# Kernel optimization log

Measured on AMD Instinct MI355X. Metric: run time of the kernel, lower is better.

## Reference

```python
import jax, jax.numpy as jnp
import numpy as np
from jax import lax

B, E, V, T = 16384, 256, 128, 16
TAU = 1.0


def _gru(x, h, Wih, Whh, bih, bhh):
    # torch.nn.GRUCell math
    gi = x @ Wih.T + bih
    gh = h @ Whh.T + bhh
    ir, iz, i_n = jnp.split(gi, 3, axis=-1)
    hr, hz, h_n = jnp.split(gh, 3, axis=-1)
    r = jax.nn.sigmoid(ir + hr)
    z = jax.nn.sigmoid(iz + hz)
    n = jnp.tanh(i_n + r * h_n)
    return (1.0 - z) * n + z * h


def setup_inputs() -> dict:
    key = jax.random.key(0)
    ks = jax.random.split(key, 10)
    s = 0.05
    w = lambda k, shape: jax.random.normal(k, shape, jnp.float32) * s
    return {
        "x": jax.random.normal(ks[0], (B, E), jnp.float32),
        "global_idxes": jnp.arange(B, dtype=jnp.int32),
        "uniform_noise": jax.random.uniform(ks[1], (T, B, V), dtype=jnp.float32),
        "dec_Wd2e": w(ks[2], (E, V)), "dec_bd2e": jnp.zeros((E,), jnp.float32),
        "dec_Wih": w(ks[3], (3 * E, E)), "dec_Whh": w(ks[4], (3 * E, E)),
        "dec_bih": jnp.zeros((3 * E,), jnp.float32), "dec_bhh": jnp.zeros((3 * E,), jnp.float32),
        "dec_We2d": w(ks[5], (V, E)), "dec_be2d": jnp.zeros((V,), jnp.float32),
        "enc_Wd2e": w(ks[6], (E, V)), "enc_bd2e": jnp.zeros((E,), jnp.float32),
        "enc_Wih": w(ks[7], (3 * E, E)), "enc_Whh": w(ks[8], (3 * E, E)),
        "enc_bih": jnp.zeros((3 * E,), jnp.float32), "enc_bhh": jnp.zeros((3 * E,), jnp.float32),
    }


def _forward(x, uniform_noise,
             dec_Wd2e, dec_bd2e, dec_Wih, dec_Whh, dec_bih, dec_bhh, dec_We2d, dec_be2d,
             enc_Wd2e, enc_bd2e, enc_Wih, enc_Whh, enc_bih, enc_bhh):
    Bn = x.shape[0]
    # gumbel noise from pre-sampled uniforms (deterministic)
    gnoise = -jnp.log(-jnp.log(uniform_noise + 1e-10) + 1e-10)  # [T,B,V]

    # ---- GumbelDecoder: sequential GRUCell decode with alive/dead masking ----
    def dec_step(carry, g_t):
        state, last_tok, alive, N, t = carry
        emb = last_tok @ dec_Wd2e.T + dec_bd2e
        state = _gru(emb, state, dec_Wih, dec_Whh, dec_bih, dec_bhh)
        logits = state @ dec_We2d.T + dec_be2d
        y_soft = jax.nn.softmax((logits + g_t) / TAU, axis=-1)
        idx = jnp.argmax(y_soft, axis=-1)
        y_hard = jax.nn.one_hot(idx, V, dtype=y_soft.dtype)
        # straight-through hard gumbel-softmax
        y = y_soft + lax.stop_gradient(y_hard - y_soft)
        ended = idx == 0  # token 0 is the terminator
        N = jnp.where(ended, jnp.minimum(N, t), N)
        alive = alive & (~ended)
        # dead rows (incl. newly ended) have their token zeroed, as in torch
        y = jnp.where(alive[:, None], y, 0.0)
        return (state, y, alive, N, t + 1), y

    init = (x, jnp.zeros((Bn, V), x.dtype), jnp.ones((Bn,), bool),
            jnp.full((Bn,), T, jnp.int32), jnp.int32(0))
    (_, _, _, N, _), utt = lax.scan(dec_step, init, gnoise)  # utt: [T,B,V]

    # ---- OnehotEncoder: sequential GRUCell encode with alive sieve (masked) ----
    def enc_step(carry, u_t):
        state, out_state, alive = carry
        emb = u_t @ enc_Wd2e.T + enc_bd2e
        state = _gru(emb, state, enc_Wih, enc_Whh, enc_bih, enc_bhh)
        out_state = jnp.where(alive[:, None], state, out_state)
        ended = u_t[:, 0] > 0.5  # terminator seen in utterance
        alive = alive & (~ended)
        return (state, out_state, alive), None

    z0 = jnp.zeros((Bn, E), x.dtype)
    (_, reconst, _), _ = lax.scan(enc_step, (z0, z0, jnp.ones((Bn,), bool)), utt)

    utterance = jnp.transpose(utt, (1, 0, 2))  # [B,T,V]
    return utterance, N, reconst


def reference(x, global_idxes, uniform_noise,
              dec_Wd2e, dec_bd2e, dec_Wih, dec_Whh, dec_bih, dec_bhh, dec_We2d, dec_be2d,
              enc_Wd2e, enc_bd2e, enc_Wih, enc_Whh, enc_bih, enc_bhh):
    del global_idxes  # unused by the original forward
    return _forward(x, uniform_noise,
                    dec_Wd2e, dec_bd2e, dec_Wih, dec_Whh, dec_bih, dec_bhh, dec_We2d, dec_be2d,
                    enc_Wd2e, enc_bd2e, enc_Wih, enc_Whh, enc_bih, enc_bhh)
```

## Files before the change

### kernel.cpp

```cpp
#include <hip/hip_runtime.h>
#include <hip/hip_bf16.h>


namespace {
constexpr int kB  = 16384;
constexpr int kE  = 256;
constexpr int kV  = 128;
constexpr int kT  = 16;
constexpr int kG3 = 768;

constexpr int kOffWdhhT  = 0;
constexpr int kOffWehhT  = kG3 * kE;
constexpr int kOffWe2dT  = 2 * kG3 * kE;
constexpr int kOffDecTab = kOffWe2dT + kV * kE;
constexpr int kOffEncTab = kOffDecTab + 129 * kG3;
}

__device__ __forceinline__ float sigmf(float v) { return 1.0f / (1.0f + expf(-v)); }
__device__ __forceinline__ float gumbelf(float u) {
  return -logf(-logf(u + 1e-10f) + 1e-10f);
}

__global__ void prep_transpose(const float* __restrict__ dWhh,
                               const float* __restrict__ eWhh,
                               const float* __restrict__ We2d,
                               float* __restrict__ ws) {
  const int n1 = kG3 * kE;
  const int n2 = n1 + kG3 * kE;
  const int n3 = n2 + kV * kE;
  for (int i = blockIdx.x * blockDim.x + threadIdx.x; i < n3;
       i += gridDim.x * blockDim.x) {
    if (i < n1) {
      const int k = i / kG3, j = i - k * kG3;
      ws[i] = dWhh[j * kE + k];
    } else if (i < n2) {
      const int t = i - n1;
      const int k = t / kG3, j = t - k * kG3;
      ws[i] = eWhh[j * kE + k];
    } else {
      const int t = i - n2;
      const int k = t / kV, v = t - k * kV;
      ws[i] = We2d[v * kE + k];
    }
  }
}

__global__ void prep_tables(const float* __restrict__ Wih,
                            const float* __restrict__ Wd2e,
                            const float* __restrict__ bd2e,
                            const float* __restrict__ bih,
                            float* __restrict__ tab) {
  const int i = blockIdx.x * blockDim.x + threadIdx.x;
  if (i >= 129 * kG3) return;
  const int v = i / kG3, j = i - v * kG3;
  const float* wr = Wih + j * kE;
  float acc = 0.0f;
  if (v < kV) {
    for (int k = 0; k < kE; ++k) acc = fmaf(wr[k], Wd2e[k * kV + v] + bd2e[k], acc);
  } else {
    for (int k = 0; k < kE; ++k) acc = fmaf(wr[k], bd2e[k], acc);
  }
  tab[i] = acc + bih[j];
}

__device__ __forceinline__ void gru_half(float acc[8][3][4],
                                         const float (*__restrict__ h)[8],
                                         const float* __restrict__ WT,
                                         const int e0) {
#pragma unroll
  for (int r = 0; r < 8; ++r)
#pragma unroll
    for (int g = 0; g < 3; ++g)
#pragma unroll
      for (int c = 0; c < 4; ++c) acc[r][g][c] = 0.0f;
#pragma unroll 2
  for (int k = 0; k < kE; ++k) {
    const float4 hA = *(const float4*)(&h[k][0]);
    const float4 hB = *(const float4*)(&h[k][4]);
    const float* wp = WT + k * kG3 + e0;
    const float4 w0 = *(const float4*)(wp);
    const float4 w1 = *(const float4*)(wp + 256);
    const float4 w2 = *(const float4*)(wp + 512);
    const float hv[8] = {hA.x, hA.y, hA.z, hA.w, hB.x, hB.y, hB.z, hB.w};
    const float wv[3][4] = {{w0.x, w0.y, w0.z, w0.w},
                            {w1.x, w1.y, w1.z, w1.w},
                            {w2.x, w2.y, w2.z, w2.w}};
#pragma unroll
    for (int r = 0; r < 8; ++r)
#pragma unroll
      for (int g = 0; g < 3; ++g)
#pragma unroll
        for (int c = 0; c < 4; ++c)
          acc[r][g][c] = fmaf(hv[r], wv[g][c], acc[r][g][c]);
  }
}

__device__ __forceinline__ void gru_pointwise(float acc[8][3][4],
                                              float (*__restrict__ h)[8],
                                              const float* __restrict__ Tab,
                                              const int tok[8],
                                              const float4& br4, const float4& bz4,
                                              const float4& bn4, const int e0) {
  const float br[4] = {br4.x, br4.y, br4.z, br4.w};
  const float bz[4] = {bz4.x, bz4.y, bz4.z, bz4.w};
  const float bn[4] = {bn4.x, bn4.y, bn4.z, bn4.w};
#pragma unroll
  for (int r = 0; r < 8; ++r) {
    const float* gp = Tab + tok[r] * kG3 + e0;
    const float4 g0 = *(const float4*)(gp);
    const float4 g1 = *(const float4*)(gp + 256);
    const float4 g2 = *(const float4*)(gp + 512);
    const float gi[3][4] = {{g0.x, g0.y, g0.z, g0.w},
                            {g1.x, g1.y, g1.z, g1.w},
                            {g2.x, g2.y, g2.z, g2.w}};
#pragma unroll
    for (int c = 0; c < 4; ++c) {
      const float rg = sigmf(gi[0][c] + acc[r][0][c] + br[c]);
      const float zg = sigmf(gi[1][c] + acc[r][1][c] + bz[c]);
      const float ng = tanhf(gi[2][c] + rg * (acc[r][2][c] + bn[c]));
      acc[r][0][c] = ng;
      acc[r][1][c] = zg;
    }
  }
#pragma unroll
  for (int c = 0; c < 4; ++c) {
    const int e = e0 + c;
    const float4 hA = *(const float4*)(&h[e][0]);
    const float4 hB = *(const float4*)(&h[e][4]);
    const float ho[8] = {hA.x, hA.y, hA.z, hA.w, hB.x, hB.y, hB.z, hB.w};
    float hn[8];
#pragma unroll
    for (int r = 0; r < 8; ++r)
      hn[r] = (1.0f - acc[r][1][c]) * acc[r][0][c] + acc[r][1][c] * ho[r];
    *(float4*)(&h[e][0]) = make_float4(hn[0], hn[1], hn[2], hn[3]);
    *(float4*)(&h[e][4]) = make_float4(hn[4], hn[5], hn[6], hn[7]);
  }
}

__launch_bounds__(256, 2)
__global__ void gumbel_fused(const float* __restrict__ x,
                             const float* __restrict__ unoise,
                             const float* __restrict__ dbhh,
                             const float* __restrict__ dbe2d,
                             const float* __restrict__ ebhh,
                             const float* __restrict__ ws,
                             float* __restrict__ out) {
  const float* WdhhT  = ws + kOffWdhhT;
  const float* WehhT  = ws + kOffWehhT;
  const float* We2dT  = ws + kOffWe2dT;
  const float* DecTab = ws + kOffDecTab;
  const float* EncTab = ws + kOffEncTab;

  __shared__ float hbuf[2][4][kE][8];

  const int tid  = (int)threadIdx.x;
  const int w    = tid >> 6;
  const int jx   = tid & 63;
  const int row0 = (int)blockIdx.x * 32 + w * 8;
  const int e0   = jx * 4;

  float (*hd)[8] = hbuf[0][w];
  float (*he)[8] = hbuf[1][w];

  for (int i = jx; i < kE * 8; i += 64) {
    const int r = i >> 8, k = i & (kE - 1);
    hd[k][r] = x[(size_t)(row0 + r) * kE + k];
    he[k][r] = 0.0f;
  }
  __syncthreads();

  int tok[8], Nn[8];
  bool alive[8];
#pragma unroll
  for (int r = 0; r < 8; ++r) { tok[r] = kV; Nn[r] = kT; alive[r] = true; }

  const float4 dbr = *(const float4*)(dbhh + e0);
  const float4 dbz = *(const float4*)(dbhh + 256 + e0);
  const float4 dbn = *(const float4*)(dbhh + 512 + e0);
  const float4 ebr = *(const float4*)(ebhh + e0);
  const float4 ebz = *(const float4*)(ebhh + 256 + e0);
  const float4 ebn = *(const float4*)(ebhh + 512 + e0);
  const float2 be2 = *(const float2*)(dbe2d + 2 * jx);

  float acc[8][3][4];

  for (int t = 0; t < kT; ++t) {
    gru_half(acc, hd, WdhhT, e0);
    gru_pointwise(acc, hd, DecTab, tok, dbr, dbz, dbn, e0);
    __syncthreads();

    float l0[8], l1[8];
#pragma unroll
    for (int r = 0; r < 8; ++r) { l0[r] = 0.0f; l1[r] = 0.0f; }
#pragma unroll 2
    for (int k = 0; k < kE; ++k) {
      const float4 hA = *(const float4*)(&hd[k][0]);
      const float4 hB = *(const float4*)(&hd[k][4]);
      const float2 wv = *(const float2*)(We2dT + k * kV + 2 * jx);
      const float hv[8] = {hA.x, hA.y, hA.z, hA.w, hB.x, hB.y, hB.z, hB.w};
#pragma unroll
      for (int r = 0; r < 8; ++r) {
        l0[r] = fmaf(hv[r], wv.x, l0[r]);
        l1[r] = fmaf(hv[r], wv.y, l1[r]);
      }
    }
    const float* up = unoise + ((size_t)t * kB + row0) * kV + 2 * jx;
#pragma unroll
    for (int r = 0; r < 8; ++r) {
      const float2 u = *(const float2*)(up + (size_t)r * kV);
      const float a0 = l0[r] + be2.x + gumbelf(u.x);
      const float a1 = l1[r] + be2.y + gumbelf(u.y);
      float mv; int mi;
      if (a1 > a0) { mv = a1; mi = 2 * jx + 1; } else { mv = a0; mi = 2 * jx; }
#pragma unroll
      for (int off = 32; off >= 1; off >>= 1) {
        const float ov = __shfl_xor(mv, off, 64);
        const int   oi = __shfl_xor(mi, off, 64);
        if (ov > mv || (ov == mv && oi < mi)) { mv = ov; mi = oi; }
      }
      const bool ended = (mi == 0);
      if (ended) Nn[r] = (Nn[r] < t) ? Nn[r] : t;
      const bool anew = alive[r] && !ended;
      alive[r] = anew;
      tok[r] = anew ? mi : kV;
      float2 pr;
      pr.x = (anew && mi == 2 * jx) ? 1.0f : 0.0f;
      pr.y = (anew && mi == 2 * jx + 1) ? 1.0f : 0.0f;
      *reinterpret_cast<float2*>(
          out + ((size_t)(row0 + r) * kT + t) * kV + 2 * jx) = pr;
    }

    gru_half(acc, he, WehhT, e0);
    gru_pointwise(acc, he, EncTab, tok, ebr, ebz, ebn, e0);
    __syncthreads();
  }

  const size_t uttN = (size_t)kB * kT * kV;
#pragma unroll
  for (int r = 0; r < 8; ++r)
    if (jx == r) out[uttN + row0 + r] = (float)Nn[r];
  for (int i = jx; i < kE * 8; i += 64) {
    const int r = i >> 8, k = i & (kE - 1);
    out[uttN + kB + (size_t)(row0 + r) * kE + k] = he[k][r];
  }
}

extern "C" void kernel_launch(void* const* d_in, const int* in_sizes, int n_in,
                              void* d_out, int out_size, void* d_ws, size_t ws_size,
                              hipStream_t stream) {
  (void)in_sizes; (void)n_in; (void)out_size; (void)ws_size;
  const float* x      = (const float*)d_in[0];
  const float* unoise = (const float*)d_in[2];
  const float* dWd2e  = (const float*)d_in[3];
  const float* dbd2e  = (const float*)d_in[4];
  const float* dWih   = (const float*)d_in[5];
  const float* dWhh   = (const float*)d_in[6];
  const float* dbih   = (const float*)d_in[7];
  const float* dbhh   = (const float*)d_in[8];
  const float* dWe2d  = (const float*)d_in[9];
  const float* dbe2d  = (const float*)d_in[10];
  const float* eWd2e  = (const float*)d_in[11];
  const float* ebd2e  = (const float*)d_in[12];
  const float* eWih   = (const float*)d_in[13];
  const float* eWhh   = (const float*)d_in[14];
  const float* ebih   = (const float*)d_in[15];
  const float* ebhh   = (const float*)d_in[16];
  float* ws = (float*)d_ws;

  prep_transpose<<<1664, 256, 0, stream>>>(dWhh, eWhh, dWe2d, ws);
  prep_tables<<<(129 * kG3 + 255) / 256, 256, 0, stream>>>(
      dWih, dWd2e, dbd2e, dbih, ws + kOffDecTab);
  prep_tables<<<(129 * kG3 + 255) / 256, 256, 0, stream>>>(
      eWih, eWd2e, ebd2e, ebih, ws + kOffEncTab);
  gumbel_fused<<<kB / 32, 256, 0, stream>>>(
      x, unoise, dbhh, dbe2d, ebhh, ws, (float*)d_out);
}
```

Before: 3.497 ms.

## Compute encoder GRU hidden matmul with split-bf16 MFMA

The encoder's recurrent h@Whh^T product now runs on bf16 MFMA instructions, using a three-way bf16 split of both operands to keep near-fp32 accuracy. A prep kernel pre-splits the encoder Whh into hi/mid/lo bf16 tables. The encoder state is held in a block-wide swizzled shared buffer, and tokens are exchanged through a scratch area in the output. This aims to offload FMA-bound work to matrix cores, at the cost of six MFMAs per product, extra global reads of the split weights, and an extra barrier per step.

```diff
diff --git a/kernel.cpp b/kernel.cpp
--- a/kernel.cpp
+++ b/kernel.cpp
@@ -1,5 +1,4 @@
 #include <hip/hip_runtime.h>
-#include <hip/hip_bf16.h>
 
 
 namespace {
@@ -10,35 +9,62 @@
 constexpr int kG3 = 768;
 
 constexpr int kOffWdhhT  = 0;
-constexpr int kOffWehhT  = kG3 * kE;
-constexpr int kOffWe2dT  = 2 * kG3 * kE;
+constexpr int kOffWe2dT  = kG3 * kE;
 constexpr int kOffDecTab = kOffWe2dT + kV * kE;
 constexpr int kOffEncTab = kOffDecTab + 129 * kG3;
-}
+constexpr int kOffBTab   = kOffEncTab + 129 * kG3;
+constexpr int kBCount    = 32 * kG3 * 8;
+}
+
+typedef short bf16x8 __attribute__((ext_vector_type(8)));
+typedef float f32x4  __attribute__((ext_vector_type(4)));
+typedef unsigned short u16;
 
 __device__ __forceinline__ float sigmf(float v) { return 1.0f / (1.0f + expf(-v)); }
 __device__ __forceinline__ float gumbelf(float u) {
   return -logf(-logf(u + 1e-10f) + 1e-10f);
 }
 
+__device__ __forceinline__ f32x4 mfma16(bf16x8 a, bf16x8 b, f32x4 c) {
+  return __builtin_amdgcn_mfma_f32_16x16x32_bf16(a, b, c, 0, 0, 0);
+}
+
+struct Bf3 { bf16x8 h, m, l; };
+
+__device__ __forceinline__ Bf3 split3(float4 a, float4 b) {
+  const float v[8] = {a.x, a.y, a.z, a.w, b.x, b.y, b.z, b.w};
+  union { bf16x8 b8; u16 u[8]; } H, M, L;
+#pragma unroll
+  for (int e = 0; e < 8; ++e) {
+    const float f = v[e];
+    const unsigned hb = __float_as_uint(f) & 0xffff0000u;
+    const float f1 = f - __uint_as_float(hb);
+    const unsigned mb = __float_as_uint(f1) & 0xffff0000u;
+    const float f2 = f1 - __uint_as_float(mb);
+    H.u[e] = (u16)(hb >> 16);
+    M.u[e] = (u16)(mb >> 16);
+    L.u[e] = (u16)(__float_as_uint(f2) >> 16);
+  }
+  Bf3 r; r.h = H.b8; r.m = M.b8; r.l = L.b8;
+  return r;
+}
+
+__device__ __forceinline__ int hidx(int row, int col) {
+  return row * kE + ((((col >> 3) ^ (row & 7)) << 3) | (col & 7));
+}
+
 __global__ void prep_transpose(const float* __restrict__ dWhh,
-                               const float* __restrict__ eWhh,
                                const float* __restrict__ We2d,
                                float* __restrict__ ws) {
   const int n1 = kG3 * kE;
-  const int n2 = n1 + kG3 * kE;
-  const int n3 = n2 + kV * kE;
-  for (int i = blockIdx.x * blockDim.x + threadIdx.x; i < n3;
+  const int n2 = n1 + kV * kE;
+  for (int i = blockIdx.x * blockDim.x + threadIdx.x; i < n2;
        i += gridDim.x * blockDim.x) {
     if (i < n1) {
       const int k = i / kG3, j = i - k * kG3;
       ws[i] = dWhh[j * kE + k];
-    } else if (i < n2) {
+    } else {
       const int t = i - n1;
-      const int k = t / kG3, j = t - k * kG3;
-      ws[i] = eWhh[j * kE + k];
-    } else {
-      const int t = i - n2;
       const int k = t / kV, v = t - k * kV;
       ws[i] = We2d[v * kE + k];
     }
@@ -63,6 +89,29 @@
   tab[i] = acc + bih[j];
 }
 
+__global__ void prep_bsplit(const float* __restrict__ eWhh,
+                            u16* __restrict__ bt) {
+  const int idx = blockIdx.x * blockDim.x + threadIdx.x;
+  if (idx >= 32 * kG3) return;
+  const int j = idx % kG3;
+  const int kg = idx / kG3;
+  u16* ph = bt + (size_t)idx * 8;
+  u16* pm = ph + kBCount;
+  u16* pl = pm + kBCount;
+  const float* src = eWhh + j * kE + kg * 8;
+#pragma unroll
+  for (int e = 0; e < 8; ++e) {
+    const float f = src[e];
+    const unsigned hb = __float_as_uint(f) & 0xffff0000u;
+    const float f1 = f - __uint_as_float(hb);
+    const unsigned mb = __float_as_uint(f1) & 0xffff0000u;
+    const float f2 = f1 - __uint_as_float(mb);
+    ph[e] = (u16)(hb >> 16);
+    pm[e] = (u16)(mb >> 16);
+    pl[e] = (u16)(__float_as_uint(f2) >> 16);
+  }
+}
+
 __device__ __forceinline__ void gru_half(float acc[8][3][4],
                                          const float (*__restrict__ h)[8],
                                          const float* __restrict__ WT,
@@ -146,27 +195,30 @@
                              const float* __restrict__ ws,
                              float* __restrict__ out) {
   const float* WdhhT  = ws + kOffWdhhT;
-  const float* WehhT  = ws + kOffWehhT;
   const float* We2dT  = ws + kOffWe2dT;
   const float* DecTab = ws + kOffDecTab;
   const float* EncTab = ws + kOffEncTab;
-
-  __shared__ float hbuf[2][4][kE][8];
+  const u16* Bh_t = (const u16*)(ws + kOffBTab);
+  const u16* Bm_t = Bh_t + kBCount;
+  const u16* Bl_t = Bh_t + 2 * kBCount;
+
+  __shared__ __align__(16) float hd_s[4][kE][8];
+  __shared__ __align__(16) float henc[32 * kE];
 
   const int tid  = (int)threadIdx.x;
   const int w    = tid >> 6;
   const int jx   = tid & 63;
-  const int row0 = (int)blockIdx.x * 32 + w * 8;
+  const int brow0 = (int)blockIdx.x * 32;
+  const int row0  = brow0 + w * 8;
   const int e0   = jx * 4;
 
-  float (*hd)[8] = hbuf[0][w];
-  float (*he)[8] = hbuf[1][w];
+  float (*hd)[8] = hd_s[w];
 
   for (int i = jx; i < kE * 8; i += 64) {
     const int r = i >> 8, k = i & (kE - 1);
     hd[k][r] = x[(size_t)(row0 + r) * kE + k];
-    he[k][r] = 0.0f;
-  }
+  }
+  for (int i = tid; i < 32 * kE; i += 256) henc[i] = 0.0f;
   __syncthreads();
 
   int tok[8], Nn[8];
@@ -177,12 +229,27 @@
   const float4 dbr = *(const float4*)(dbhh + e0);
   const float4 dbz = *(const float4*)(dbhh + 256 + e0);
   const float4 dbn = *(const float4*)(dbhh + 512 + e0);
-  const float4 ebr = *(const float4*)(ebhh + e0);
-  const float4 ebz = *(const float4*)(ebhh + 256 + e0);
-  const float4 ebn = *(const float4*)(ebhh + 512 + e0);
   const float2 be2 = *(const float2*)(dbe2d + 2 * jx);
 
+  const int l15  = jx & 15;
+  const int ksub = jx >> 4;
+  const int arow0 = l15, arow1 = l15 + 16;
+  const int a0base = arow0 * kE, a1base = arow1 * kE;
+  const int a0m7 = arow0 & 7, a1m7 = arow1 & 7;
+  float ebr[4], ebz[4], ebn[4];
+#pragma unroll
+  for (int nn = 0; nn < 4; ++nn) {
+    const int ec = (w << 6) + (nn << 4) + l15;
+    ebr[nn] = ebhh[ec];
+    ebz[nn] = ebhh[kE + ec];
+    ebn[nn] = ebhh[2 * kE + ec];
+  }
+
+  const size_t uttN = (size_t)kB * kT * kV;
+  int* tokg = (int*)(out + uttN);
+
   float acc[8][3][4];
+  const f32x4 zero4 = {0.0f, 0.0f, 0.0f, 0.0f};
 
   for (int t = 0; t < kT; ++t) {
     gru_half(acc, hd, WdhhT, e0);
@@ -223,6 +290,7 @@
       const bool anew = alive[r] && !ended;
       alive[r] = anew;
       tok[r] = anew ? mi : kV;
+      if (jx == r) tokg[row0 + r] = tok[r];
       float2 pr;
       pr.x = (anew && mi == 2 * jx) ? 1.0f : 0.0f;
       pr.y = (anew && mi == 2 * jx + 1) ? 1.0f : 0.0f;
@@ -230,18 +298,73 @@
           out + ((size_t)(row0 + r) * kT + t) * kV + 2 * jx) = pr;
     }
 
-    gru_half(acc, he, WehhT, e0);
-    gru_pointwise(acc, he, EncTab, tok, ebr, ebz, ebn, e0);
+    f32x4 eacc[2][12];
+#pragma unroll
+    for (int m = 0; m < 2; ++m)
+#pragma unroll
+      for (int nt = 0; nt < 12; ++nt) eacc[m][nt] = zero4;
+
+#pragma unroll 2
+    for (int kt = 0; kt < 8; ++kt) {
+      const int c0 = ((kt << 2) + ksub) ^ a0m7;
+      const int c1 = ((kt << 2) + ksub) ^ a1m7;
+      const float4 f00 = *(const float4*)&henc[a0base + (c0 << 3)];
+      const float4 f01 = *(const float4*)&henc[a0base + (c0 << 3) + 4];
+      const float4 f10 = *(const float4*)&henc[a1base + (c1 << 3)];
+      const float4 f11 = *(const float4*)&henc[a1base + (c1 << 3) + 4];
+      const Bf3 A0 = split3(f00, f01);
+      const Bf3 A1 = split3(f10, f11);
+      const int recb = (((kt << 2) + ksub) * kG3 + (w << 6) + l15) * 8;
+#pragma unroll
+      for (int nt = 0; nt < 12; ++nt) {
+        const int off = recb + ((nt >> 2) * 256 + (nt & 3) * 16) * 8;
+        const bf16x8 Bh = *reinterpret_cast<const bf16x8*>(Bh_t + off);
+        const bf16x8 Bm = *reinterpret_cast<const bf16x8*>(Bm_t + off);
+        const bf16x8 Bl = *reinterpret_cast<const bf16x8*>(Bl_t + off);
+        eacc[0][nt] = mfma16(A0.h, Bh, eacc[0][nt]);
+        eacc[1][nt] = mfma16(A1.h, Bh, eacc[1][nt]);
+        eacc[0][nt] = mfma16(A0.h, Bm, eacc[0][nt]);
+        eacc[1][nt] = mfma16(A1.h, Bm, eacc[1][nt]);
+        eacc[0][nt] = mfma16(A0.m, Bh, eacc[0][nt]);
+        eacc[1][nt] = mfma16(A1.m, Bh, eacc[1][nt]);
+        eacc[0][nt] = mfma16(A0.h, Bl, eacc[0][nt]);
+        eacc[1][nt] = mfma16(A1.h, Bl, eacc[1][nt]);
+        eacc[0][nt] = mfma16(A0.l, Bh, eacc[0][nt]);
+        eacc[1][nt] = mfma16(A1.l, Bh, eacc[1][nt]);
+        eacc[0][nt] = mfma16(A0.m, Bm, eacc[0][nt]);
+        eacc[1][nt] = mfma16(A1.m, Bm, eacc[1][nt]);
+      }
+    }
     __syncthreads();
-  }
-
-  const size_t uttN = (size_t)kB * kT * kV;
+
+#pragma unroll
+    for (int m = 0; m < 2; ++m) {
+#pragma unroll
+      for (int j2 = 0; j2 < 4; ++j2) {
+        const int row = (m << 4) + (ksub << 2) + j2;
+        const int tk = tokg[brow0 + row];
+        const float* gp = EncTab + tk * kG3;
+#pragma unroll
+        for (int nn = 0; nn < 4; ++nn) {
+          const int ec = (w << 6) + (nn << 4) + l15;
+          const float rg = sigmf(gp[ec] + eacc[m][nn][j2] + ebr[nn]);
+          const float zg = sigmf(gp[kE + ec] + eacc[m][4 + nn][j2] + ebz[nn]);
+          const float ng = tanhf(gp[2 * kE + ec] + rg * (eacc[m][8 + nn][j2] + ebn[nn]));
+          const int hx = hidx(row, ec);
+          const float ho = henc[hx];
+          henc[hx] = (1.0f - zg) * ng + zg * ho;
+        }
+      }
+    }
+    __syncthreads();
+  }
+
 #pragma unroll
   for (int r = 0; r < 8; ++r)
     if (jx == r) out[uttN + row0 + r] = (float)Nn[r];
-  for (int i = jx; i < kE * 8; i += 64) {
-    const int r = i >> 8, k = i & (kE - 1);
-    out[uttN + kB + (size_t)(row0 + r) * kE + k] = he[k][r];
+  for (int i = tid; i < 32 * kE; i += 256) {
+    const int row = i >> 8, col = i & (kE - 1);
+    out[uttN + kB + (size_t)(brow0 + row) * kE + col] = henc[hidx(row, col)];
   }
 }
 
@@ -267,11 +390,13 @@
   const float* ebhh   = (const float*)d_in[16];
   float* ws = (float*)d_ws;
 
-  prep_transpose<<<1664, 256, 0, stream>>>(dWhh, eWhh, dWe2d, ws);
+  prep_transpose<<<896, 256, 0, stream>>>(dWhh, dWe2d, ws);
   prep_tables<<<(129 * kG3 + 255) / 256, 256, 0, stream>>>(
       dWih, dWd2e, dbd2e, dbih, ws + kOffDecTab);
   prep_tables<<<(129 * kG3 + 255) / 256, 256, 0, stream>>>(
       eWih, eWd2e, ebd2e, ebih, ws + kOffEncTab);
+  prep_bsplit<<<(32 * kG3 + 255) / 256, 256, 0, stream>>>(
+      eWhh, (u16*)(ws + kOffBTab));
   gumbel_fused<<<kB / 32, 256, 0, stream>>>(
       x, unoise, dbhh, dbe2d, ebhh, ws, (float*)d_out);
 }
```

Result: slower. 3.630 ms (+3.8%).
